# Optimization experiments

Measured on AMD Instinct MI355X. Metric: run time of the kernel, lower is better.

The kernel has to match this reference:

```python
import jax, jax.numpy as jnp
import numpy as np

RES_SCALE = 0.1
B, C, H, W = 16, 256, 96, 96


def conv3x3(x, w):
    # NCHW input, OIHW weight, SAME padding (padding=1 for k=3), no bias
    return jax.lax.conv_general_dilated(
        x, w, window_strides=(1, 1), padding="SAME",
        dimension_numbers=("NCHW", "OIHW", "NCHW"))


def setup_inputs() -> dict:
    key = jax.random.key(0)
    k1, k2, k3, k4 = jax.random.split(key, 4)
    fan = C * 9
    x = jax.random.normal(k1, (B, C, H, W), dtype=jnp.float32)
    conv2_w = jax.random.normal(k2, (C, C, 3, 3), dtype=jnp.float32) / np.sqrt(fan)
    conv3_w = jax.random.normal(k3, (C, C, 3, 3), dtype=jnp.float32) / np.sqrt(fan)
    prelu_w = jnp.full((1,), 0.25, dtype=jnp.float32)  # nn.PReLU default init
    # interleaved channel partition: P=0::3 (86), R=1::3 (85), T=2::3 (85)
    idx_p = jnp.arange(0, C, 3, dtype=jnp.int32)
    idx_r = jnp.arange(1, C, 3, dtype=jnp.int32)
    idx_t = jnp.arange(2, C, 3, dtype=jnp.int32)
    return {"x": x, "conv2_w": conv2_w, "conv3_w": conv3_w, "prelu_w": prelu_w,
            "idx_p": idx_p, "idx_r": idx_r, "idx_t": idx_t}


def reference(x, conv2_w, conv3_w, prelu_w, idx_p, idx_r, idx_t):
    # op2 = conv2(prune(x, skip_gate)) ; all-ones gate -> identity prune
    op2 = conv3x3(x, conv2_w)  # [B, C, H, W]
    # per-channel activation routing (gathers permute channel order to [P,R,T])
    gp = op2[:, idx_p]                                  # [B, 86, H, W]
    a = jnp.concatenate([
        jnp.where(gp >= 0, gp, prelu_w[0] * gp),        # PReLU (1 shared param)
        jax.nn.relu(op2[:, idx_r]),                     # [B, 85, H, W]
        jnp.tanh(op2[:, idx_t]),                        # [B, 85, H, W]
    ], axis=1)                                          # [B, C, H, W]
    # conv_tot branch: op3 = conv3(a)*res_scale + x * reshape(skip_conv_gate)
    # skip_conv_gate == ones here, so the skip scaling is identity
    op3 = conv3x3(a, conv3_w) * RES_SCALE + x
    return op3


if __name__ == "__main__":
    out = reference(**setup_inputs())
    print(out.shape, out.dtype)
```

## Files before the change

### kernel.cpp

```cpp
#include <hip/hip_runtime.h>
#include <math.h>


#define Bn 16
#define Cn 256
#define Hn 96
#define Wn 96
#define PH 98
#define PW 98
#define HW (Hn*Wn)

typedef __bf16 bf16x8 __attribute__((ext_vector_type(8)));
typedef float  f32x4  __attribute__((ext_vector_type(4)));

__device__ __forceinline__ unsigned short f2bf(float f) {
    unsigned int u = __float_as_uint(f);
    unsigned int r = (u + 0x7fffu + ((u >> 16) & 1u)) >> 16;
    return (unsigned short)r;
}

__device__ __forceinline__ void lds_load16(void* lds, const void* g) {
    auto gp = (const __attribute__((address_space(1))) char*)(unsigned long long)(uintptr_t)g;
    auto lp = (__attribute__((address_space(3))) char*)(unsigned int)(uintptr_t)lds;
    __builtin_amdgcn_global_load_lds(gp, lp, 16, 0, 0);
}

#define SB() __builtin_amdgcn_sched_barrier(0)
#define MEMFENCE() asm volatile("" ::: "memory")

__global__ __launch_bounds__(256)
void zero_border_k(unsigned short* __restrict__ t) {
    int idx = blockIdx.x * 256 + threadIdx.x;
    int oct = idx & 31;
    int rest = idx >> 5;
    int pidx = rest % 388;
    int b = rest / 388;
    int h, w;
    if (pidx < 98)       { h = 0;  w = pidx; }
    else if (pidx < 196) { h = 97; w = pidx - 98; }
    else if (pidx < 292) { h = pidx - 196 + 1; w = 0; }
    else                 { h = pidx - 292 + 1; w = 97; }
    size_t e = ((size_t)(b * PH + h) * PW + w) * 256 + oct * 8;
    *(uint4*)(t + e) = make_uint4(0u, 0u, 0u, 0u);
}

template<bool PERM>
__global__ __launch_bounds__(256)
void pack_w_k(const float* __restrict__ w, unsigned short* __restrict__ wp) {
    int idx = blockIdx.x * 256 + threadIdx.x;
    int ci_l = idx & 31;
    int c    = (idx >> 5) & 255;
    int v    = idx >> 13;
    int k9   = v % 9;
    int cc   = v / 9;
    int co;
    if (PERM) {
        co = (c < 86) ? c * 3 : (c < 171) ? (c - 86) * 3 + 1 : (c - 171) * 3 + 2;
    } else {
        co = c;
    }
    float val = w[((size_t)co * 256 + cc * 32 + ci_l) * 9 + k9];
    wp[idx] = f2bf(val);
}

__global__ __launch_bounds__(256)
void transform_x_k(const float* __restrict__ x, unsigned short* __restrict__ xp) {
    __shared__ float s[32 * 33];
    const int t = threadIdx.x;
    const int col0 = blockIdx.x * 32;
    const int row  = blockIdx.y;
    const int z = blockIdx.z;
    const int b = z >> 3;
    const int ci0 = (z & 7) * 32;

    #pragma unroll
    for (int i = 0; i < 4; ++i) {
        int ci = i * 8 + (t >> 5);
        int px = t & 31;
        s[ci * 33 + px] = x[((size_t)(b * Cn + ci0 + ci)) * HW + row * Wn + col0 + px];
    }
    __syncthreads();
    const int px = t >> 3;
    const int c4 = (t & 7) * 4;
    ushort4 o;
    o.x = f2bf(s[(c4 + 0) * 33 + px]);
    o.y = f2bf(s[(c4 + 1) * 33 + px]);
    o.z = f2bf(s[(c4 + 2) * 33 + px]);
    o.w = f2bf(s[(c4 + 3) * 33 + px]);
    size_t e = ((size_t)(b * PH + row + 1) * PW + (col0 + px + 1)) * 256 + ci0 + c4;
    *(ushort4*)(xp + e) = o;
}

template<int MODE>
__global__ __launch_bounds__(512) __attribute__((amdgpu_waves_per_eu(2, 2)))
void conv_k(const unsigned short* __restrict__ in_cl,
            const unsigned short* __restrict__ wp,
            const float* __restrict__ prelu_w,
            const float* __restrict__ xres,
            void* __restrict__ outp)
{
    __shared__ unsigned short s_x[2][2048 * 8];
    __shared__ unsigned short s_w[2][1536 * 8];

    const int tid = threadIdx.x;
    const int bid = blockIdx.x;
    const int wg = (bid & 7) * 96 + (bid >> 3);
    const int blk_co = (wg & 1) * 128;
    const int t2 = wg >> 1;
    const int tile = t2 % 24;
    const int b = t2 / 24;
    const int R0 = (tile / 3) * 12;
    const int C0 = (tile % 3) * 32;

    const int lane = tid & 63;
    const int wv = tid >> 6;
    const int l15 = lane & 15;
    const int qq = lane >> 4;
    const int cg = wv & 1;
    const int wrow = wv >> 1;
    const int qa = qq ^ ((l15 >> 1) & 3);

    const unsigned short* img = in_cl + (size_t)b * PH * PW * 256;

    int xg[4];
    #pragma unroll
    for (int i = 0; i < 4; ++i) {
        int slot = i * 512 + tid;
        int lsl = slot ^ ((slot >> 3) & 3);
        if (lsl > 1903) lsl = 1903;
        int p = lsl >> 2;
        int pr = p / 34, pc = p - pr * 34;
        xg[i] = ((R0 + pr) * PW + (C0 + pc)) * 256 + (lsl & 3) * 8;
    }
    int wbase[3];
    #pragma unroll
    for (int i = 0; i < 3; ++i) {
        int slot = i * 512 + tid;
        int lsl = slot ^ ((slot >> 3) & 3);
        int kw = lsl >> 9;
        int co = (lsl >> 2) & 127;
        wbase[i] = kw * 8192 + (blk_co + co) * 32 + (lsl & 3) * 8;
    }

    f32x4 acc[4][6];
    #pragma unroll
    for (int m = 0; m < 4; ++m)
        #pragma unroll
        for (int n = 0; n < 6; ++n) acc[m][n] = 0.f;

    #pragma unroll
    for (int i = 0; i < 3; ++i) lds_load16(&s_w[0][(size_t)(i * 512 + tid) * 8], wp + wbase[i]);
    #pragma unroll
    for (int i = 0; i < 4; ++i) lds_load16(&s_x[0][(size_t)(i * 512 + tid) * 8], img + xg[i]);
    MEMFENCE(); SB();
    asm volatile("s_waitcnt vmcnt(0)" ::: "memory");
    SB();
    __builtin_amdgcn_s_barrier();
    SB();

    for (int s = 0; s < 24; ++s) {
        const int c  = s / 3;
        const int kh = s - 3 * c;
        const unsigned short* swc = s_w[s & 1];
        const unsigned short* sxc = s_x[c & 1];

        #pragma unroll
        for (int kw = 0; kw < 3; ++kw) {
            bf16x8 af[4], bf[6];
            #pragma unroll
            for (int m = 0; m < 4; ++m) {
                const int row_ = kw * 128 + cg * 64 + m * 16 + l15;
                af[m] = *(const bf16x8*)&swc[row_ * 32 + qa * 8];
            }
            #pragma unroll
            for (int n = 0; n < 6; ++n) {
                const int P_ = (wrow * 3 + (n >> 1) + kh) * 34 + (n & 1) * 16 + l15 + kw;
                bf[n] = *(const bf16x8*)&sxc[P_ * 32 + ((qq ^ ((P_ >> 1) & 3)) << 3)];
            }
            if (s < 23)
                lds_load16(&s_w[(s + 1) & 1][(size_t)(kw * 512 + tid) * 8],
                           wp + (size_t)(s + 1) * 24576 + wbase[kw]);
            if (c < 7) {
                if (kh == 1)
                    lds_load16(&s_x[(c + 1) & 1][(size_t)(kw * 512 + tid) * 8],
                               img + xg[kw] + (c + 1) * 32);
                else if (kh == 2 && kw == 0)
                    lds_load16(&s_x[(c + 1) & 1][(size_t)(3 * 512 + tid) * 8],
                               img + xg[3] + (c + 1) * 32);
            }
            MEMFENCE(); SB();
            __builtin_amdgcn_s_barrier();
            asm volatile("s_waitcnt lgkmcnt(0)" ::: "memory");
            SB();
            __builtin_amdgcn_s_setprio(1);
            #pragma unroll
            for (int n = 0; n < 6; ++n)
                #pragma unroll
                for (int m = 0; m < 4; ++m)
                    acc[m][n] = __builtin_amdgcn_mfma_f32_16x16x32_bf16(af[m], bf[n], acc[m][n], 0, 0, 0);
            __builtin_amdgcn_s_setprio(0);
            SB();
            if (kw == 2) {
                if (kh == 1 && c < 7)
                    asm volatile("s_waitcnt vmcnt(1)" ::: "memory");
                else
                    asm volatile("s_waitcnt vmcnt(0)" ::: "memory");
                SB();
            }
            __builtin_amdgcn_s_barrier();
        }
    }

    if constexpr (MODE == 0) {
        const float pw = prelu_w[0];
        unsigned short* aout = (unsigned short*)outp;
        #pragma unroll
        for (int n = 0; n < 6; ++n) {
            const int row_p = wrow * 3 + (n >> 1);
            const int col_p = (n & 1) * 16 + l15;
            size_t pix = ((size_t)(b * PH + R0 + row_p + 1)) * PW + (C0 + col_p + 1);
            #pragma unroll
            for (int m = 0; m < 4; ++m) {
                const int cb = blk_co + cg * 64 + m * 16 + qq * 4;
                float r[4];
                #pragma unroll
                for (int j = 0; j < 4; ++j) {
                    const int ch = cb + j;
                    float s = acc[m][n][j];
                    if (ch < 86)        r[j] = s >= 0.f ? s : pw * s;
                    else if (ch < 171)  r[j] = fmaxf(s, 0.f);
                    else {
                        float e = __expf(2.f * s);
                        r[j] = 1.f - 2.f / (e + 1.f);
                    }
                }
                ushort4 o;
                o.x = f2bf(r[0]); o.y = f2bf(r[1]); o.z = f2bf(r[2]); o.w = f2bf(r[3]);
                *(ushort4*)(aout + pix * 256 + cb) = o;
            }
        }
    } else {
        float* fout = (float*)outp;
        #pragma unroll
        for (int n = 0; n < 6; ++n) {
            const int row_p = wrow * 3 + (n >> 1);
            const int col_p = (n & 1) * 16 + l15;
            #pragma unroll
            for (int m = 0; m < 4; ++m) {
                const int cb = blk_co + cg * 64 + m * 16 + qq * 4;
                size_t base = ((size_t)(b * Cn + cb)) * HW + (size_t)(R0 + row_p) * Wn + (C0 + col_p);
                #pragma unroll
                for (int j = 0; j < 4; ++j)
                    fout[base + (size_t)j * HW] = acc[m][n][j] * 0.1f + xres[base + (size_t)j * HW];
            }
        }
    }
}

extern "C" void kernel_launch(void* const* d_in, const int* in_sizes, int n_in,
                              void* d_out, int out_size, void* d_ws, size_t ws_size,
                              hipStream_t stream) {
    const float* x  = (const float*)d_in[0];
    const float* w2 = (const float*)d_in[1];
    const float* w3 = (const float*)d_in[2];
    const float* pw = (const float*)d_in[3];
    float* out = (float*)d_out;
    char* ws = (char*)d_ws;

    unsigned short* a_cl = (unsigned short*)ws;
    unsigned short* wp2  = (unsigned short*)(ws + 78675968);
    unsigned short* wp3  = (unsigned short*)(ws + 78675968 + 1179648);
    unsigned short* x_pad = (unsigned short*)d_out;

    zero_border_k<<<776, 256, 0, stream>>>(x_pad);
    zero_border_k<<<776, 256, 0, stream>>>(a_cl);
    pack_w_k<true ><<<2304, 256, 0, stream>>>(w2, wp2);
    pack_w_k<false><<<2304, 256, 0, stream>>>(w3, wp3);
    transform_x_k<<<dim3(3, 96, 128), 256, 0, stream>>>(x, x_pad);

    conv_k<0><<<768, 512, 0, stream>>>(x_pad, wp2, pw, nullptr, (void*)a_cl);
    conv_k<1><<<768, 512, 0, stream>>>(a_cl, wp3, nullptr, x, (void*)out);
}
```

Baseline: 438.5 us.

## Shrink conv workgroup tile to 64 channels x 8x32 pixels for occupancy

The implicit-GEMM conv kernel goes from 512-thread blocks (128 output channels, 12x32 pixels, 6 MFMA columns per wave) to 256-thread blocks (64 channels, 8x32 pixels, 4x4 MFMAs per wave) with four blocks per CU and 2304 blocks in total. The activation tile is now single-buffered and reloaded once per 32-channel chunk. Weights are double-buffered per kernel tap with a barrier every tap. This targets occupancy and latency hiding through more waves, but each block reuses less data, issues more global loads for the input halo and weights, synchronises more often, and stalls on every activation reload.

```diff
diff --git a/kernel.cpp b/kernel.cpp
--- a/kernel.cpp
+++ b/kernel.cpp
@@ -92,136 +92,129 @@
 }
 
 template<int MODE>
-__global__ __launch_bounds__(512) __attribute__((amdgpu_waves_per_eu(2, 2)))
+__global__ __launch_bounds__(256, 4)
 void conv_k(const unsigned short* __restrict__ in_cl,
             const unsigned short* __restrict__ wp,
             const float* __restrict__ prelu_w,
             const float* __restrict__ xres,
             void* __restrict__ outp)
 {
-    __shared__ unsigned short s_x[2][2048 * 8];
-    __shared__ unsigned short s_w[2][1536 * 8];
+    __shared__ unsigned short s_x[1536 * 8];
+    __shared__ unsigned short s_w[2][256 * 8];
 
     const int tid = threadIdx.x;
     const int bid = blockIdx.x;
-    const int wg = (bid & 7) * 96 + (bid >> 3);
-    const int blk_co = (wg & 1) * 128;
-    const int t2 = wg >> 1;
-    const int tile = t2 % 24;
-    const int b = t2 / 24;
-    const int R0 = (tile / 3) * 12;
+    const int wg = (bid & 7) * 288 + (bid >> 3);
+    const int co_base = (wg & 3) * 64;
+    const int t2 = wg >> 2;
+    const int tile = t2 % 36;
+    const int b = t2 / 36;
+    const int R0 = (tile / 3) * 8;
     const int C0 = (tile % 3) * 32;
 
     const int lane = tid & 63;
     const int wv = tid >> 6;
     const int l15 = lane & 15;
     const int qq = lane >> 4;
-    const int cg = wv & 1;
-    const int wrow = wv >> 1;
     const int qa = qq ^ ((l15 >> 1) & 3);
 
     const unsigned short* img = in_cl + (size_t)b * PH * PW * 256;
 
-    int xg[4];
-    #pragma unroll
-    for (int i = 0; i < 4; ++i) {
-        int slot = i * 512 + tid;
+    int xg[6];
+    #pragma unroll
+    for (int i = 0; i < 6; ++i) {
+        int slot = i * 256 + tid;
         int lsl = slot ^ ((slot >> 3) & 3);
-        if (lsl > 1903) lsl = 1903;
+        if (lsl > 1359) lsl = 1359;
         int p = lsl >> 2;
         int pr = p / 34, pc = p - pr * 34;
         xg[i] = ((R0 + pr) * PW + (C0 + pc)) * 256 + (lsl & 3) * 8;
     }
-    int wbase[3];
-    #pragma unroll
-    for (int i = 0; i < 3; ++i) {
-        int slot = i * 512 + tid;
-        int lsl = slot ^ ((slot >> 3) & 3);
-        int kw = lsl >> 9;
-        int co = (lsl >> 2) & 127;
-        wbase[i] = kw * 8192 + (blk_co + co) * 32 + (lsl & 3) * 8;
-    }
-
-    f32x4 acc[4][6];
+    int wroff;
+    {
+        int lsl = tid ^ ((tid >> 3) & 3);
+        wroff = (co_base + (lsl >> 2)) * 32 + (lsl & 3) * 8;
+    }
+
+    f32x4 acc[4][4];
     #pragma unroll
     for (int m = 0; m < 4; ++m)
         #pragma unroll
-        for (int n = 0; n < 6; ++n) acc[m][n] = 0.f;
-
-    #pragma unroll
-    for (int i = 0; i < 3; ++i) lds_load16(&s_w[0][(size_t)(i * 512 + tid) * 8], wp + wbase[i]);
-    #pragma unroll
-    for (int i = 0; i < 4; ++i) lds_load16(&s_x[0][(size_t)(i * 512 + tid) * 8], img + xg[i]);
+        for (int n = 0; n < 4; ++n) acc[m][n] = 0.f;
+
+    lds_load16(&s_w[0][(size_t)tid * 8], wp + wroff);
+    #pragma unroll
+    for (int i = 0; i < 6; ++i)
+        lds_load16(&s_x[(size_t)(i * 256 + tid) * 8], img + xg[i]);
     MEMFENCE(); SB();
     asm volatile("s_waitcnt vmcnt(0)" ::: "memory");
     SB();
     __builtin_amdgcn_s_barrier();
     SB();
 
-    for (int s = 0; s < 24; ++s) {
-        const int c  = s / 3;
-        const int kh = s - 3 * c;
-        const unsigned short* swc = s_w[s & 1];
-        const unsigned short* sxc = s_x[c & 1];
-
-        #pragma unroll
-        for (int kw = 0; kw < 3; ++kw) {
-            bf16x8 af[4], bf[6];
-            #pragma unroll
-            for (int m = 0; m < 4; ++m) {
-                const int row_ = kw * 128 + cg * 64 + m * 16 + l15;
-                af[m] = *(const bf16x8*)&swc[row_ * 32 + qa * 8];
-            }
-            #pragma unroll
-            for (int n = 0; n < 6; ++n) {
-                const int P_ = (wrow * 3 + (n >> 1) + kh) * 34 + (n & 1) * 16 + l15 + kw;
-                bf[n] = *(const bf16x8*)&sxc[P_ * 32 + ((qq ^ ((P_ >> 1) & 3)) << 3)];
-            }
-            if (s < 23)
-                lds_load16(&s_w[(s + 1) & 1][(size_t)(kw * 512 + tid) * 8],
-                           wp + (size_t)(s + 1) * 24576 + wbase[kw]);
-            if (c < 7) {
-                if (kh == 1)
-                    lds_load16(&s_x[(c + 1) & 1][(size_t)(kw * 512 + tid) * 8],
-                               img + xg[kw] + (c + 1) * 32);
-                else if (kh == 2 && kw == 0)
-                    lds_load16(&s_x[(c + 1) & 1][(size_t)(3 * 512 + tid) * 8],
-                               img + xg[3] + (c + 1) * 32);
-            }
+    for (int c = 0; c < 8; ++c) {
+        #pragma unroll
+        for (int k9 = 0; k9 < 9; ++k9) {
+            const int s = c * 9 + k9;
+            const int kh = k9 / 3, kw = k9 - 3 * kh;
+            const unsigned short* swc = s_w[s & 1];
+
+            if (c < 7 || k9 < 8)
+                lds_load16(&s_w[(s + 1) & 1][(size_t)tid * 8],
+                           wp + (size_t)(s + 1) * 8192 + wroff);
             MEMFENCE(); SB();
-            __builtin_amdgcn_s_barrier();
-            asm volatile("s_waitcnt lgkmcnt(0)" ::: "memory");
-            SB();
+
+            bf16x8 af[4], bf[4];
+            #pragma unroll
+            for (int m = 0; m < 4; ++m)
+                af[m] = *(const bf16x8*)&swc[(m * 16 + l15) * 32 + qa * 8];
+            #pragma unroll
+            for (int n = 0; n < 4; ++n) {
+                const int P = (wv * 2 + (n >> 1) + kh) * 34 + (n & 1) * 16 + l15 + kw;
+                bf[n] = *(const bf16x8*)&s_x[P * 32 + ((qq ^ ((P >> 1) & 3)) << 3)];
+            }
             __builtin_amdgcn_s_setprio(1);
             #pragma unroll
-            for (int n = 0; n < 6; ++n)
+            for (int n = 0; n < 4; ++n)
                 #pragma unroll
                 for (int m = 0; m < 4; ++m)
                     acc[m][n] = __builtin_amdgcn_mfma_f32_16x16x32_bf16(af[m], bf[n], acc[m][n], 0, 0, 0);
             __builtin_amdgcn_s_setprio(0);
             SB();
-            if (kw == 2) {
-                if (kh == 1 && c < 7)
-                    asm volatile("s_waitcnt vmcnt(1)" ::: "memory");
-                else
-                    asm volatile("s_waitcnt vmcnt(0)" ::: "memory");
+
+            if (k9 < 8) {
+                asm volatile("s_waitcnt vmcnt(0)" ::: "memory");
                 SB();
-            }
-            __builtin_amdgcn_s_barrier();
-        }
+                __builtin_amdgcn_s_barrier();
+                SB();
+            }
+        }
+        __builtin_amdgcn_s_barrier();
+        SB();
+        if (c < 7) {
+            #pragma unroll
+            for (int i = 0; i < 6; ++i)
+                lds_load16(&s_x[(size_t)(i * 256 + tid) * 8],
+                           img + xg[i] + (c + 1) * 32);
+            MEMFENCE(); SB();
+        }
+        asm volatile("s_waitcnt vmcnt(0)" ::: "memory");
+        SB();
+        __builtin_amdgcn_s_barrier();
+        SB();
     }
 
     if constexpr (MODE == 0) {
         const float pw = prelu_w[0];
         unsigned short* aout = (unsigned short*)outp;
         #pragma unroll
-        for (int n = 0; n < 6; ++n) {
-            const int row_p = wrow * 3 + (n >> 1);
+        for (int n = 0; n < 4; ++n) {
+            const int row_p = wv * 2 + (n >> 1);
             const int col_p = (n & 1) * 16 + l15;
             size_t pix = ((size_t)(b * PH + R0 + row_p + 1)) * PW + (C0 + col_p + 1);
             #pragma unroll
             for (int m = 0; m < 4; ++m) {
-                const int cb = blk_co + cg * 64 + m * 16 + qq * 4;
+                const int cb = co_base + m * 16 + qq * 4;
                 float r[4];
                 #pragma unroll
                 for (int j = 0; j < 4; ++j) {
@@ -242,12 +235,12 @@
     } else {
         float* fout = (float*)outp;
         #pragma unroll
-        for (int n = 0; n < 6; ++n) {
-            const int row_p = wrow * 3 + (n >> 1);
+        for (int n = 0; n < 4; ++n) {
+            const int row_p = wv * 2 + (n >> 1);
             const int col_p = (n & 1) * 16 + l15;
             #pragma unroll
             for (int m = 0; m < 4; ++m) {
-                const int cb = blk_co + cg * 64 + m * 16 + qq * 4;
+                const int cb = co_base + m * 16 + qq * 4;
                 size_t base = ((size_t)(b * Cn + cb)) * HW + (size_t)(R0 + row_p) * Wn + (C0 + col_p);
                 #pragma unroll
                 for (int j = 0; j < 4; ++j)
@@ -278,6 +271,6 @@
     pack_w_k<false><<<2304, 256, 0, stream>>>(w3, wp3);
     transform_x_k<<<dim3(3, 96, 128), 256, 0, stream>>>(x, x_pad);
 
-    conv_k<0><<<768, 512, 0, stream>>>(x_pad, wp2, pw, nullptr, (void*)a_cl);
-    conv_k<1><<<768, 512, 0, stream>>>(a_cl, wp3, nullptr, x, (void*)out);
-}
+    conv_k<0><<<2304, 256, 0, stream>>>(x_pad, wp2, pw, nullptr, (void*)a_cl);
+    conv_k<1><<<2304, 256, 0, stream>>>(a_cl, wp3, nullptr, x, (void*)out);
+}
```

Result: no change. 433.8 us (-1.1%).
